# Kernel tuning notes

Hardware: AMD Instinct MI355X
Metric: run time of the kernel (lower is better)

The kernel has to match this reference:

```python
import jax, jax.numpy as jnp
import numpy as np

B, IN, OUT, Q = 2048, 1024, 1024, 16

def setup_inputs() -> dict:
    key = jax.random.key(0)
    k1, k2, k3, k4 = jax.random.split(key, 4)
    bound = 1.0 / np.sqrt(IN)
    x = jax.random.normal(k1, (B, IN), dtype=jnp.float32)
    indices = jax.random.randint(k2, (B, IN), 0, Q, dtype=jnp.int32)
    # param_index: per-(quantile, input-feature) weight vector of length size_out
    param_table = jax.random.uniform(k3, (Q, IN, OUT), dtype=jnp.float32,
                                     minval=-bound, maxval=bound)
    bias = jax.random.uniform(k4, (OUT,), dtype=jnp.float32,
                              minval=-bound, maxval=bound)
    return {"x": x, "indices": indices, "param_table": param_table,
            "bias": bias, "store_activations": 0, "get_indices": 0, "use_db": 0}

def reference(x, indices, param_table, bias, store_activations, get_indices, use_db):
    # out[b, o] = sum_i param_table[indices[b,i], i, o] * x[b,i]  + bias[o]
    # Expressed as Q masked matmuls to avoid a [B, IN, OUT] gathered intermediate:
    # route each (b, i) contribution to its quantile's weight slab.
    q = param_table.shape[0]
    onehot = jax.nn.one_hot(indices, q, dtype=x.dtype)      # [B, IN, Q]
    xq = onehot * x[..., None]                               # [B, IN, Q]
    w_times_x = jnp.einsum('biq,qio->bo', xq, param_table)   # [B, OUT]
    return w_times_x + bias
```

## Files before the change

### kernel.cpp

```cpp
#include <hip/hip_runtime.h>
#include <stdint.h>

#define B_SZ   2048
#define IN_SZ  1024
#define OUT_SZ 1024
#define Q_SZ   16
#define NZB    4

typedef __attribute__((ext_vector_type(8))) short short8;
typedef __attribute__((ext_vector_type(4))) float floatx4;
typedef __attribute__((ext_vector_type(2))) unsigned short u16x2;
typedef __attribute__((ext_vector_type(2))) short s16x2;

__device__ __forceinline__ unsigned short f32_to_bf16_rne(float f) {
    union { float f; uint32_t u; } v; v.f = f;
    uint32_t u = v.u;
    return (unsigned short)((u + 0x7FFFu + ((u >> 16) & 1u)) >> 16);
}

__device__ __forceinline__ uint32_t mask3(uint32_t xv, uint32_t ohv, unsigned short sh) {
    union { uint32_t u; u16x2 v; s16x2 s; } t;
    t.u = ohv;
    u16x2 shv; shv.x = sh; shv.y = sh;
    t.v = t.v << shv;
    s16x2 f15; f15.x = 15; f15.y = 15;
    t.s = t.s >> f15;
    return xv & t.u;
}

__device__ __forceinline__ void gload_lds16(const void* g, void* l) {
    __builtin_amdgcn_global_load_lds(
        (const __attribute__((address_space(1))) unsigned int*)g,
        (__attribute__((address_space(3))) unsigned int*)l, 16, 0, 0);
}

__global__ void k_build_wf(const float* __restrict__ W, unsigned short* __restrict__ Wf) {
    const int S = blockIdx.x;
    const int q = S & 15, ih = (S >> 4) & 3, xb = (S >> 6) & 7, zb = S >> 9;
    const int t = threadIdx.x;
    const int i0 = zb * 256 + ih * 64;
    const int o0 = xb * 128;
    __shared__ unsigned short lds[64][130];

#pragma unroll
    for (int it = 0; it < 8; ++it) {
        int r  = it * 8 + (t >> 5);
        int c4 = (t & 31) * 4;
        float4 v = *(const float4*)(W + ((size_t)(q * 1024 + i0 + r)) * 1024 + o0 + c4);
        unsigned short h0 = f32_to_bf16_rne(v.x), h1 = f32_to_bf16_rne(v.y);
        unsigned short h2 = f32_to_bf16_rne(v.z), h3 = f32_to_bf16_rne(v.w);
        *(uint32_t*)&lds[r][c4]     = (uint32_t)h0 | ((uint32_t)h1 << 16);
        *(uint32_t*)&lds[r][c4 + 2] = (uint32_t)h2 | ((uint32_t)h3 << 16);
    }
    __syncthreads();

    unsigned short* dst = Wf + (size_t)S * 8192;
#pragma unroll
    for (int it = 0; it < 4; ++it) {
        int c = it * 256 + t;
        int L = c & 63;
        int hnt = c >> 6;
        int h = hnt >> 3, nt = hnt & 7;
        int ol = nt * 16 + (L & 15);
        int il = h * 32 + (L >> 4) * 8;
        unsigned short v[8];
#pragma unroll
        for (int j = 0; j < 8; ++j) v[j] = lds[il + j][ol];
        *(uint4*)(dst + (size_t)c * 8) = *(uint4*)v;
    }
}

__global__ __launch_bounds__(256, 2) void k_gemm(const unsigned short* __restrict__ Wf,
                                                 const float* __restrict__ x,
                                                 const int* __restrict__ idx,
                                                 float* __restrict__ P) {
    const int tid  = threadIdx.x;
    const int wave = tid >> 6, lane = tid & 63;
    const int hord = (wave >> 1) & 1;

    const int id = blockIdx.x;
    const int zb = id & 3;
    const int xb = (id >> 2) & 7;
    const int yb = id >> 5;
    const int o0 = xb * 128, b0 = yb * 128, ibase = zb * 256;

    const char* wbase = (const char*)Wf + (size_t)(zb * 8 + xb) * 64 * 16384;
    const int   lofs  = lane * 16;

    const int aoff0 = hord * 32,   aoff1 = 32 - aoff0;
    const int boff0 = hord * 8192, boff1 = 8192 - boff0;

    __shared__ unsigned char sm[4][16384];

    const int arow = b0 + wave * 32 + (lane & 15);
    const float* xg = x + (size_t)arow * IN_SZ + ibase + (lane >> 4) * 8;
    const int*   ig = idx + (size_t)arow * IN_SZ + ibase + (lane >> 4) * 8;

    floatx4 acc[16];
#pragma unroll
    for (int i = 0; i < 16; ++i) acc[i] = (floatx4){0.f, 0.f, 0.f, 0.f};

    uint4 xr[2][2], oh[2][2];
    short8 fc[8], fn[8];

#define RELOADA(ih)                                                           \
    {   int io_ = (ih) * 64;                                                  \
        _Pragma("unroll")                                                     \
        for (int mt_ = 0; mt_ < 2; ++mt_)                                     \
            _Pragma("unroll")                                                 \
            for (int sl_ = 0; sl_ < 2; ++sl_) {                               \
                const int ao_ = (sl_ == 0) ? aoff0 : aoff1;                   \
                const float* xp_ = xg + mt_ * 16 * IN_SZ + io_ + ao_;         \
                const int*   ip_ = ig + mt_ * 16 * IN_SZ + io_ + ao_;         \
                float a_[8]; int b_[8];                                       \
                *(float4*)(a_)     = *(const float4*)xp_;                     \
                *(float4*)(a_ + 4) = *((const float4*)xp_ + 1);               \
                *(int4*)(b_)       = *(const int4*)ip_;                       \
                *(int4*)(b_ + 4)   = *((const int4*)ip_ + 1);                 \
                unsigned short xv_[8];                                        \
                _Pragma("unroll")                                             \
                for (int j_ = 0; j_ < 8; ++j_) xv_[j_] = f32_to_bf16_rne(a_[j_]); \
                xr[mt_][sl_] = *(uint4*)xv_;                                  \
                uint32_t iw_[4];                                              \
                _Pragma("unroll")                                             \
                for (int w_ = 0; w_ < 4; ++w_)                                \
                    iw_[w_] = (1u << b_[2 * w_]) | ((1u << b_[2 * w_ + 1]) << 16); \
                oh[mt_][sl_] = *(uint4*)iw_;                                  \
            }                                                                 \
    }

#define MASKS(sl)                                                             \
        _Pragma("unroll")                                                     \
        for (int mt_ = 0; mt_ < 2; ++mt_) {                                   \
            aF[mt_].u.x = mask3(xr[mt_][sl].x, oh[mt_][sl].x, sh_);           \
            aF[mt_].u.y = mask3(xr[mt_][sl].y, oh[mt_][sl].y, sh_);           \
            aF[mt_].u.z = mask3(xr[mt_][sl].z, oh[mt_][sl].z, sh_);           \
            aF[mt_].u.w = mask3(xr[mt_][sl].w, oh[mt_][sl].w, sh_);           \
        }

    const int soff = wave * 4096 + lofs;
#define STAGE(s_, r_)                                                         \
    {   const char* gp_ = wbase + (size_t)(s_) * 16384 + soff;                \
        unsigned char* lp_ = (unsigned char*)sm + (r_) * 16384 + soff;        \
        gload_lds16(gp_,        lp_);                                         \
        gload_lds16(gp_ + 1024, lp_ + 1024);                                  \
        gload_lds16(gp_ + 2048, lp_ + 2048);                                  \
        gload_lds16(gp_ + 3072, lp_ + 3072);                                  \
    }

#define DSREAD(dst, rr, hofs)                                                 \
    {   const unsigned char* bp_ = (const unsigned char*)sm + (rr) * 16384 +  \
                                   (hofs) + lofs;                             \
        _Pragma("unroll")                                                     \
        for (int nt_ = 0; nt_ < 8; ++nt_)                                     \
            (dst)[nt_] = *(const short8*)(bp_ + nt_ * 1024);                  \
    }

#define MFMA16(fa)                                                            \
        __builtin_amdgcn_s_setprio(1);                                        \
        _Pragma("unroll")                                                     \
        for (int mt_ = 0; mt_ < 2; ++mt_)                                     \
            _Pragma("unroll")                                                 \
            for (int nt_ = 0; nt_ < 8; ++nt_)                                 \
                acc[mt_ * 8 + nt_] = __builtin_amdgcn_mfma_f32_16x16x32_bf16( \
                    aF[mt_].s8, (fa)[nt_], acc[mt_ * 8 + nt_], 0, 0, 0);      \
        __builtin_amdgcn_s_setprio(0);

#define SLAB(s_, rc_, rn_, rs_)                                               \
    {   if ((s_) < 62) STAGE((s_) + 2, rs_);                                  \
        DSREAD(fn, rc_, boff1);                                               \
        const unsigned short sh_ = (unsigned short)(15 - ((s_) & 15));        \
        union { uint4 u; short8 s8; } aF[2];                                  \
        MASKS(0);                                                             \
        MFMA16(fc);                                                           \
        if ((s_) < 63) DSREAD(fc, rn_, boff0);                                \
        MASKS(1);                                                             \
        MFMA16(fn);                                                           \
        __syncthreads();                                                      \
    }

    RELOADA(0);
    STAGE(0, 0);
    STAGE(1, 1);
    __syncthreads();
    DSREAD(fc, 0, boff0);

#pragma unroll 1
    for (int gg = 0; gg < 16; ++gg) {
        if (gg && (gg & 3) == 0) RELOADA(gg >> 2);
        const int s0 = gg * 4;
        SLAB(s0 + 0, 0, 1, 2);
        SLAB(s0 + 1, 1, 2, 3);
        SLAB(s0 + 2, 2, 3, 0);
        SLAB(s0 + 3, 3, 0, 1);
    }

    float* Pz = P + (size_t)zb * (B_SZ * OUT_SZ);
    int cn = lane & 15, rq = lane >> 4;
#pragma unroll
    for (int mt = 0; mt < 2; ++mt)
#pragma unroll
        for (int nt = 0; nt < 8; ++nt) {
            int bb = b0 + wave * 32 + mt * 16 + rq * 4;
            int oo = o0 + nt * 16 + cn;
#pragma unroll
            for (int e = 0; e < 4; ++e)
                Pz[(size_t)(bb + e) * OUT_SZ + oo] = acc[mt * 8 + nt][e];
        }
#undef RELOADA
#undef MASKS
#undef STAGE
#undef DSREAD
#undef MFMA16
#undef SLAB
}

__global__ void k_reduce(const float* __restrict__ P, const float* __restrict__ bias,
                         float* __restrict__ out) {
    int t = blockIdx.x * 256 + threadIdx.x;
    const float4* b4 = (const float4*)bias;
    float4 a = b4[t & 255];
#pragma unroll
    for (int z = 0; z < NZB; ++z) {
        float4 v = ((const float4*)P)[(size_t)z * (B_SZ * OUT_SZ / 4) + t];
        a.x += v.x; a.y += v.y; a.z += v.z; a.w += v.w;
    }
    ((float4*)out)[t] = a;
}

__global__ void k_naive(const float* __restrict__ x, const int* __restrict__ idx,
                        const float* __restrict__ W, const float* __restrict__ bias,
                        float* __restrict__ out) {
    int b = blockIdx.x;
    int o = threadIdx.x * 4;
    float4 acc = *(const float4*)(bias + o);
    const float* xr = x + (size_t)b * IN_SZ;
    const int*   ir = idx + (size_t)b * IN_SZ;
    for (int i = 0; i < IN_SZ; ++i) {
        float xv = xr[i];
        int q = ir[i];
        float4 w4 = *(const float4*)(W + ((size_t)q * IN_SZ + i) * OUT_SZ + o);
        acc.x += xv * w4.x; acc.y += xv * w4.y;
        acc.z += xv * w4.z; acc.w += xv * w4.w;
    }
    *(float4*)(out + (size_t)b * OUT_SZ + o) = acc;
}

extern "C" void kernel_launch(void* const* d_in, const int* in_sizes, int n_in,
                              void* d_out, int out_size, void* d_ws, size_t ws_size,
                              hipStream_t stream) {
    const float* x    = (const float*)d_in[0];
    const int*   idx  = (const int*)d_in[1];
    const float* W    = (const float*)d_in[2];
    const float* bias = (const float*)d_in[3];
    float* out = (float*)d_out;

    const size_t wf_bytes = (size_t)2048 * 16384;
    const size_t p_bytes  = (size_t)NZB * B_SZ * OUT_SZ * 4;
    if (ws_size < wf_bytes + p_bytes) {
        k_naive<<<dim3(B_SZ), dim3(256), 0, stream>>>(x, idx, W, bias, out);
        return;
    }
    unsigned short* Wf = (unsigned short*)d_ws;
    float* P = (float*)((char*)d_ws + wf_bytes);

    k_build_wf<<<dim3(2048), dim3(256), 0, stream>>>(W, Wf);
    k_gemm<<<dim3(NZB * 8 * (B_SZ / 128)), dim3(256), 0, stream>>>(Wf, x, idx, P);
    k_reduce<<<dim3(2048), dim3(256), 0, stream>>>(P, bias, out);
}
```

Before: 185.2 us.

## Process two W slabs per barrier with per-wave staggered half-slab order

The main loop now handles two staged weight slabs between __syncthreads instead of one, staging two slabs ahead at a time, which halves the number of block barriers. Each wave walks the four half-slabs in a rotated order (phase = wave & 3), with the quantile shift adjusted per phase. This spreads LDS bank traffic and A-mask work across waves and removes the carried prefetch register set. In exchange it needs more precomputed offsets and changes how the four-buffer ring is used, so the prefetch distance per barrier gets shorter.

```diff
diff --git a/kernel.cpp b/kernel.cpp
--- a/kernel.cpp
+++ b/kernel.cpp
@@ -76,7 +76,6 @@
                                                  float* __restrict__ P) {
     const int tid  = threadIdx.x;
     const int wave = tid >> 6, lane = tid & 63;
-    const int hord = (wave >> 1) & 1;
 
     const int id = blockIdx.x;
     const int zb = id & 3;
@@ -87,8 +86,19 @@
     const char* wbase = (const char*)Wf + (size_t)(zb * 8 + xb) * 64 * 16384;
     const int   lofs  = lane * 16;
 
-    const int aoff0 = hord * 32,   aoff1 = 32 - aoff0;
-    const int boff0 = hord * 8192, boff1 = 8192 - boff0;
+    const int ph0 = wave & 3, ph1 = (wave + 1) & 3,
+              ph2 = (wave + 2) & 3, ph3 = (wave + 3) & 3;
+    const int sel0 = ph0 >> 1, sel1 = ph1 >> 1, sel2 = ph2 >> 1, sel3 = ph3 >> 1;
+    const int hh0 = ph0 & 1, hh1 = ph1 & 1, hh2 = ph2 & 1, hh3 = ph3 & 1;
+    const int bo0_0 = ((0 + sel0) & 3) * 16384 + hh0 * 8192 + lofs;
+    const int bo1_0 = ((0 + sel1) & 3) * 16384 + hh1 * 8192 + lofs;
+    const int bo2_0 = ((0 + sel2) & 3) * 16384 + hh2 * 8192 + lofs;
+    const int bo3_0 = ((0 + sel3) & 3) * 16384 + hh3 * 8192 + lofs;
+    const int bo0_2 = ((2 + sel0) & 3) * 16384 + hh0 * 8192 + lofs;
+    const int bo1_2 = ((2 + sel1) & 3) * 16384 + hh1 * 8192 + lofs;
+    const int bo2_2 = ((2 + sel2) & 3) * 16384 + hh2 * 8192 + lofs;
+    const int bo3_2 = ((2 + sel3) & 3) * 16384 + hh3 * 8192 + lofs;
+    const int aoff0 = (wave & 1) * 32, aoff1 = 32 - aoff0;
 
     __shared__ unsigned char sm[4][16384];
 
@@ -101,7 +111,7 @@
     for (int i = 0; i < 16; ++i) acc[i] = (floatx4){0.f, 0.f, 0.f, 0.f};
 
     uint4 xr[2][2], oh[2][2];
-    short8 fc[8], fn[8];
+    short8 fA[8], fB[8];
 
 #define RELOADA(ih)                                                           \
     {   int io_ = (ih) * 64;                                                  \
@@ -129,13 +139,13 @@
             }                                                                 \
     }
 
-#define MASKS(sl)                                                             \
+#define MASKSP(par, shv)                                                      \
         _Pragma("unroll")                                                     \
         for (int mt_ = 0; mt_ < 2; ++mt_) {                                   \
-            aF[mt_].u.x = mask3(xr[mt_][sl].x, oh[mt_][sl].x, sh_);           \
-            aF[mt_].u.y = mask3(xr[mt_][sl].y, oh[mt_][sl].y, sh_);           \
-            aF[mt_].u.z = mask3(xr[mt_][sl].z, oh[mt_][sl].z, sh_);           \
-            aF[mt_].u.w = mask3(xr[mt_][sl].w, oh[mt_][sl].w, sh_);           \
+            aF[mt_].u.x = mask3(xr[mt_][par].x, oh[mt_][par].x, shv);         \
+            aF[mt_].u.y = mask3(xr[mt_][par].y, oh[mt_][par].y, shv);         \
+            aF[mt_].u.z = mask3(xr[mt_][par].z, oh[mt_][par].z, shv);         \
+            aF[mt_].u.w = mask3(xr[mt_][par].w, oh[mt_][par].w, shv);         \
         }
 
     const int soff = wave * 4096 + lofs;
@@ -148,9 +158,8 @@
         gload_lds16(gp_ + 3072, lp_ + 3072);                                  \
     }
 
-#define DSREAD(dst, rr, hofs)                                                 \
-    {   const unsigned char* bp_ = (const unsigned char*)sm + (rr) * 16384 +  \
-                                   (hofs) + lofs;                             \
+#define DSREAD(dst, boff)                                                     \
+    {   const unsigned char* bp_ = (const unsigned char*)sm + (boff);         \
         _Pragma("unroll")                                                     \
         for (int nt_ = 0; nt_ < 8; ++nt_)                                     \
             (dst)[nt_] = *(const short8*)(bp_ + nt_ * 1024);                  \
@@ -166,16 +175,26 @@
                     aF[mt_].s8, (fa)[nt_], acc[mt_ * 8 + nt_], 0, 0, 0);      \
         __builtin_amdgcn_s_setprio(0);
 
-#define SLAB(s_, rc_, rn_, rs_)                                               \
-    {   if ((s_) < 62) STAGE((s_) + 2, rs_);                                  \
-        DSREAD(fn, rc_, boff1);                                               \
-        const unsigned short sh_ = (unsigned short)(15 - ((s_) & 15));        \
+#define PAIR(s0_, bo0_, bo1_, bo2_, bo3_, dostage_, st2_, st3_)               \
+    {   if (dostage_) { STAGE((s0_) + 2, st2_); STAGE((s0_) + 3, st3_); }     \
+        const int q0_ = (s0_) & 15;                                           \
+        const unsigned short sv0_ = (unsigned short)(15 - q0_ - sel0);        \
+        const unsigned short sv1_ = (unsigned short)(15 - q0_ - sel1);        \
+        const unsigned short sv2_ = (unsigned short)(15 - q0_ - sel2);        \
+        const unsigned short sv3_ = (unsigned short)(15 - q0_ - sel3);        \
         union { uint4 u; short8 s8; } aF[2];                                  \
-        MASKS(0);                                                             \
-        MFMA16(fc);                                                           \
-        if ((s_) < 63) DSREAD(fc, rn_, boff0);                                \
-        MASKS(1);                                                             \
-        MFMA16(fn);                                                           \
+        DSREAD(fA, bo0_);                                                     \
+        MASKSP(0, sv0_);                                                      \
+        DSREAD(fB, bo1_);                                                     \
+        MFMA16(fA);                                                           \
+        MASKSP(1, sv1_);                                                      \
+        DSREAD(fA, bo2_);                                                     \
+        MFMA16(fB);                                                           \
+        MASKSP(0, sv2_);                                                      \
+        DSREAD(fB, bo3_);                                                     \
+        MFMA16(fA);                                                           \
+        MASKSP(1, sv3_);                                                      \
+        MFMA16(fB);                                                           \
         __syncthreads();                                                      \
     }
 
@@ -183,16 +202,13 @@
     STAGE(0, 0);
     STAGE(1, 1);
     __syncthreads();
-    DSREAD(fc, 0, boff0);
 
 #pragma unroll 1
     for (int gg = 0; gg < 16; ++gg) {
         if (gg && (gg & 3) == 0) RELOADA(gg >> 2);
-        const int s0 = gg * 4;
-        SLAB(s0 + 0, 0, 1, 2);
-        SLAB(s0 + 1, 1, 2, 3);
-        SLAB(s0 + 2, 2, 3, 0);
-        SLAB(s0 + 3, 3, 0, 1);
+        const int s0 = 4 * gg;
+        PAIR(s0,     bo0_0, bo1_0, bo2_0, bo3_0, 1,       2, 3);
+        PAIR(s0 + 2, bo0_2, bo1_2, bo2_2, bo3_2, gg < 15, 0, 1);
     }
 
     float* Pz = P + (size_t)zb * (B_SZ * OUT_SZ);
@@ -208,11 +224,11 @@
                 Pz[(size_t)(bb + e) * OUT_SZ + oo] = acc[mt * 8 + nt][e];
         }
 #undef RELOADA
-#undef MASKS
+#undef MASKSP
 #undef STAGE
 #undef DSREAD
 #undef MFMA16
-#undef SLAB
+#undef PAIR
 }
 
 __global__ void k_reduce(const float* __restrict__ P, const float* __restrict__ bias,
```

Measured after the change: 184.4 us. No clear change (-0.4%).
